# Optimization experiments

Measured on AMD Instinct MI355X. Metric: run time of the kernel, lower is better.

## Reference

```python
import jax, jax.numpy as jnp
import numpy as np

BLOCK = 8
SCALE = 0.5  # deterministic choice from scale_factors=[0.5, 0.75]


def setup_inputs() -> dict:
    key = jax.random.key(0)
    k1, k2 = jax.random.split(key)
    B, C, H, W = 32, 3, 512, 512
    x = jax.random.uniform(k1, (B, C, H, W), dtype=jnp.float32) * 2.0 - 1.0  # images in [-1,1]
    # per-8x8-block uniform values u in [0,1); noise = (u - 0.5)/50
    block_noise = jax.random.uniform(k2, (B, H // BLOCK, W // BLOCK), dtype=jnp.float32)
    return {"x": x, "block_noise": block_noise}


def reference(x, block_noise):
    B, C, H, W = x.shape
    nH, nW = int(H * SCALE), int(W * SCALE)
    # bilinear down then up, half-pixel centers == torch align_corners=False
    x_ds = jax.image.resize(x, (B, C, nH, nW), method="bilinear")
    x_rec = jax.image.resize(x_ds, (B, C, H, W), method="bilinear")
    # block noise: one scalar per 8x8 block, broadcast over channels
    noise = (block_noise - 0.5) / 50.0  # [B, H/8, W/8]
    noise_full = jnp.repeat(jnp.repeat(noise, BLOCK, axis=1), BLOCK, axis=2)  # [B, H, W]
    out = jnp.clip(x_rec + noise_full[:, None, :, :], -1.0, 1.0)
    return out
```

## Files before the change

kernel.cpp:

```cpp
#include <hip/hip_runtime.h>


typedef float f32x4 __attribute__((ext_vector_type(4)));

namespace {
constexpr int IMG = 512;
constexpr int TY = 8;
constexpr int HROWS = TY + 6;
constexpr float I32 = 1.0f / 32.0f;
constexpr float I7  = 1.0f / 7.0f;
constexpr float I28 = 1.0f / 28.0f;
}

__device__ __forceinline__ f32x4 vfma(float w, f32x4 a, f32x4 acc) {
  acc.x = fmaf(w, a.x, acc.x); acc.y = fmaf(w, a.y, acc.y);
  acc.z = fmaf(w, a.z, acc.z); acc.w = fmaf(w, a.w, acc.w);
  return acc;
}
__device__ __forceinline__ f32x4 vmul(float w, f32x4 a) {
  f32x4 r; r.x = w * a.x; r.y = w * a.y; r.z = w * a.z; r.w = w * a.w;
  return r;
}

__global__ __launch_bounds__(512) void compress_fused6_kernel(
    const float* __restrict__ x, const float* __restrict__ bn,
    float* __restrict__ out) {
  const int nwg = gridDim.x;
  const int cpx = nwg >> 3;
  const int bid = blockIdx.x;
  const int logical = (bid & 7) * cpx + (bid >> 3);
  const int ty = logical & 63;
  const int plane = logical >> 6;
  const int b = plane / 3;
  const int y0 = ty * TY;
  const int tid = threadIdx.x;
  const int cg = tid & 127;
  const int rs = tid >> 7;
  const int gx0 = 4 * cg;

  __shared__ float H[HROWS][IMG];

  const float* xp = x + (size_t)plane * (IMG * IMG);
  float* op = out + (size_t)plane * (IMG * IMG);

  const float nzv =
      (bn[(size_t)b * 4096 + (y0 >> 3) * 64 + (cg >> 1)] - 0.5f) * 0.02f;

  const bool left  = (cg == 0);
  const bool right = (cg == 127);
  const int A0 = left ? 0 : (right ? IMG - 12 : gx0 - 4);

  auto rowptr = [&](int r) -> const f32x4* {
    int g = y0 - 3 + r;
    g = max(0, min(IMG - 1, g));
    return (const f32x4*)(xp + (size_t)g * IMG + A0);
  };

  f32x4 qa, qb, qc;
  { const f32x4* p = rowptr(rs); qa = p[0]; qb = p[1]; qc = p[2]; }

#pragma unroll
  for (int k = 0; k < 4; ++k) {
    const int r = rs + 4 * k;
    const int rn = r + 4;
    f32x4 na, nb, nc;
    if (rn < HROWS) { const f32x4* p = rowptr(rn); na = p[0]; nb = p[1]; nc = p[2]; }
    if (r < HROWS) {
      const float f0 = qa.x, f1 = qa.y, f2 = qa.z, f3 = qa.w;
      const float f4_ = qb.x, f5 = qb.y, f6 = qb.z, f7 = qb.w;
      const float f8 = qc.x, f9 = qc.y, f10 = qc.z, f11 = qc.w;
      f32x4 h;
      if (left) {
        h.x = (3.f * f0 + 3.f * f1 + f2) * I7;
        h.y = 9*I28*f0 + (9*I28 + I32)*f1 + (3*I28 + 3*I32)*f2 + 3*I32*f3 + I32*f4_;
        h.z = 3*I28*f0 + (3*I28 + 3*I32)*f1 + (I28 + 9*I32)*f2 + 9*I32*f3 + 3*I32*f4_;
        h.w = (3.f*f1 + 9.f*f2 + 10.f*f3 + 6.f*f4_ + 3.f*f5 + f6) * I32;
      } else if (right) {
        h.x = (f5 + 3.f*f6 + 6.f*f7 + 10.f*f8 + 9.f*f9 + 3.f*f10) * I32;
        h.y = 3*I32*f7 + 9*I32*f8 + (I28 + 9*I32)*f9 + (3*I28 + 3*I32)*f10 + 3*I28*f11;
        h.z = I32*f7 + 3*I32*f8 + (3*I28 + 3*I32)*f9 + (9*I28 + I32)*f10 + 9*I28*f11;
        h.w = (f9 + 3.f*f10 + 3.f*f11) * I7;
      } else {
        h.x = (f1 + 3.f*f2 + 6.f*f3 + 10.f*f4_ + 9.f*f5 + 3.f*f6) * I32;
        h.y = (3.f*f3 + 9.f*f4_ + 10.f*f5 + 6.f*f6 + 3.f*f7 + f8) * I32;
        h.z = (f3 + 3.f*f4_ + 6.f*f5 + 10.f*f6 + 9.f*f7 + 3.f*f8) * I32;
        h.w = (3.f*f5 + 9.f*f6 + 10.f*f7 + 6.f*f8 + 3.f*f9 + f10) * I32;
      }
      *(f32x4*)&H[r][gx0] = h;
    }
    if (rn < HROWS) { qa = na; qb = nb; qc = nc; }
  }
  __syncthreads();

  const int wb = 2 * rs;
  const bool top = (y0 == 0);
  const bool bot = (y0 == IMG - TY);
  const int gy0 = y0 + 2 * rs;

#define LDQ(j) (*(const f32x4*)&H[wb + (j)][gx0])
  const f32x4 q0 = LDQ(0), q1 = LDQ(1), q2 = LDQ(2), q3 = LDQ(3);
  const f32x4 q4 = LDQ(4), q5 = LDQ(5), q6 = LDQ(6), q7 = LDQ(7);
#undef LDQ

  f32x4 oE, oO;
  if (top && rs == 0) {
    oE = vfma(3*I7, q3, vfma(3*I7, q4, vmul(I7, q5)));
    oO = vfma(9*I28, q3, vfma(9*I28 + I32, q4,
         vfma(3*I28 + 3*I32, q5, vfma(3*I32, q6, vmul(I32, q7)))));
  } else if (top && rs == 1) {
    oE = vfma(3*I28, q1, vfma(3*I28 + 3*I32, q2,
         vfma(I28 + 9*I32, q3, vfma(9*I32, q4, vmul(3*I32, q5)))));
    oO = vfma(3*I32, q2, vfma(9*I32, q3, vfma(10*I32, q4,
         vfma(6*I32, q5, vfma(3*I32, q6, vmul(I32, q7))))));
  } else if (bot && rs == 2) {
    oE = vfma(I32, q0, vfma(3*I32, q1, vfma(6*I32, q2,
         vfma(10*I32, q3, vfma(9*I32, q4, vmul(3*I32, q5))))));
    oO = vfma(3*I32, q2, vfma(9*I32, q3, vfma(I28 + 9*I32, q4,
         vfma(3*I28 + 3*I32, q5, vmul(3*I28, q6)))));
  } else if (bot && rs == 3) {
    oE = vfma(I32, q0, vfma(3*I32, q1, vfma(3*I28 + 3*I32, q2,
         vfma(9*I28 + I32, q3, vmul(9*I28, q4)))));
    oO = vfma(I7, q2, vfma(3*I7, q3, vmul(3*I7, q4)));
  } else {
    oE = vfma(I32, q0, vfma(3*I32, q1, vfma(6*I32, q2,
         vfma(10*I32, q3, vfma(9*I32, q4, vmul(3*I32, q5))))));
    oO = vfma(3*I32, q2, vfma(9*I32, q3, vfma(10*I32, q4,
         vfma(6*I32, q5, vfma(3*I32, q6, vmul(I32, q7))))));
  }

#define FINISH_STORE(o, ii)                                                    \
  {                                                                            \
    f32x4 v = o;                                                               \
    v.x = fminf(1.f, fmaxf(-1.f, v.x + nzv));                                  \
    v.y = fminf(1.f, fmaxf(-1.f, v.y + nzv));                                  \
    v.z = fminf(1.f, fmaxf(-1.f, v.z + nzv));                                  \
    v.w = fminf(1.f, fmaxf(-1.f, v.w + nzv));                                  \
    __builtin_nontemporal_store(v, (f32x4*)(op + (size_t)(gy0 + ii) * IMG + gx0)); \
  }
  FINISH_STORE(oE, 0)
  FINISH_STORE(oO, 1)
#undef FINISH_STORE
}

extern "C" void kernel_launch(void* const* d_in, const int* in_sizes, int n_in,
                              void* d_out, int out_size, void* d_ws, size_t ws_size,
                              hipStream_t stream) {
  const float* x  = (const float*)d_in[0];
  const float* bn = (const float*)d_in[1];
  float* out = (float*)d_out;

  const int n_planes = in_sizes[0] / (IMG * IMG);
  const int nwg = (IMG / TY) * n_planes;
  compress_fused6_kernel<<<dim3(nwg), dim3(512), 0, stream>>>(x, bn, out);
}
```

Before: 37.22 us.

## Double row tile to 16 with 1024-thread blocks and batched halo loads

Raises the output rows per workgroup from 8 to 16 and the block size from 512 to 1024 threads. The 6-row vertical halo is now amortized over twice as many output rows, which cuts redundant global reads and horizontal-pass work. The software-pipelined row loop is replaced by up to three row loads issued per thread before the horizontal convolution, and the noise index is recomputed per row group. The trade-offs are half as many workgroups, a larger shared tile, and higher register pressure under the 1024-thread launch bound.

Result: slower. 38.31 us (+2.9%).

```diff
diff --git a/kernel.cpp b/kernel.cpp
--- a/kernel.cpp
+++ b/kernel.cpp
@@ -5,7 +5,7 @@
 
 namespace {
 constexpr int IMG = 512;
-constexpr int TY = 8;
+constexpr int TY = 16;
 constexpr int HROWS = TY + 6;
 constexpr float I32 = 1.0f / 32.0f;
 constexpr float I7  = 1.0f / 7.0f;
@@ -22,15 +22,15 @@
   return r;
 }
 
-__global__ __launch_bounds__(512) void compress_fused6_kernel(
+__global__ __launch_bounds__(1024, 8) void compress_fused7_kernel(
     const float* __restrict__ x, const float* __restrict__ bn,
     float* __restrict__ out) {
   const int nwg = gridDim.x;
   const int cpx = nwg >> 3;
   const int bid = blockIdx.x;
   const int logical = (bid & 7) * cpx + (bid >> 3);
-  const int ty = logical & 63;
-  const int plane = logical >> 6;
+  const int ty = logical & 31;
+  const int plane = logical >> 5;
   const int b = plane / 3;
   const int y0 = ty * TY;
   const int tid = threadIdx.x;
@@ -44,7 +44,7 @@
   float* op = out + (size_t)plane * (IMG * IMG);
 
   const float nzv =
-      (bn[(size_t)b * 4096 + (y0 >> 3) * 64 + (cg >> 1)] - 0.5f) * 0.02f;
+      (bn[(size_t)b * 4096 + ((y0 + 2 * rs) >> 3) * 64 + (cg >> 1)] - 0.5f) * 0.02f;
 
   const bool left  = (cg == 0);
   const bool right = (cg == 127);
@@ -56,40 +56,43 @@
     return (const f32x4*)(xp + (size_t)g * IMG + A0);
   };
 
-  f32x4 qa, qb, qc;
-  { const f32x4* p = rowptr(rs); qa = p[0]; qb = p[1]; qc = p[2]; }
+  auto hconv = [&](f32x4 qa, f32x4 qb, f32x4 qc) -> f32x4 {
+    const float f0 = qa.x, f1 = qa.y, f2 = qa.z, f3 = qa.w;
+    const float f4_ = qb.x, f5 = qb.y, f6 = qb.z, f7 = qb.w;
+    const float f8 = qc.x, f9 = qc.y, f10 = qc.z, f11 = qc.w;
+    f32x4 h;
+    if (left) {
+      h.x = (3.f * f0 + 3.f * f1 + f2) * I7;
+      h.y = 9*I28*f0 + (9*I28 + I32)*f1 + (3*I28 + 3*I32)*f2 + 3*I32*f3 + I32*f4_;
+      h.z = 3*I28*f0 + (3*I28 + 3*I32)*f1 + (I28 + 9*I32)*f2 + 9*I32*f3 + 3*I32*f4_;
+      h.w = (3.f*f1 + 9.f*f2 + 10.f*f3 + 6.f*f4_ + 3.f*f5 + f6) * I32;
+    } else if (right) {
+      h.x = (f5 + 3.f*f6 + 6.f*f7 + 10.f*f8 + 9.f*f9 + 3.f*f10) * I32;
+      h.y = 3*I32*f7 + 9*I32*f8 + (I28 + 9*I32)*f9 + (3*I28 + 3*I32)*f10 + 3*I28*f11;
+      h.z = I32*f7 + 3*I32*f8 + (3*I28 + 3*I32)*f9 + (9*I28 + I32)*f10 + 9*I28*f11;
+      h.w = (f9 + 3.f*f10 + 3.f*f11) * I7;
+    } else {
+      h.x = (f1 + 3.f*f2 + 6.f*f3 + 10.f*f4_ + 9.f*f5 + 3.f*f6) * I32;
+      h.y = (3.f*f3 + 9.f*f4_ + 10.f*f5 + 6.f*f6 + 3.f*f7 + f8) * I32;
+      h.z = (f3 + 3.f*f4_ + 6.f*f5 + 10.f*f6 + 9.f*f7 + 3.f*f8) * I32;
+      h.w = (3.f*f5 + 9.f*f6 + 10.f*f7 + 6.f*f8 + 3.f*f9 + f10) * I32;
+    }
+    return h;
+  };
 
-#pragma unroll
-  for (int k = 0; k < 4; ++k) {
-    const int r = rs + 4 * k;
-    const int rn = r + 4;
-    f32x4 na, nb, nc;
-    if (rn < HROWS) { const f32x4* p = rowptr(rn); na = p[0]; nb = p[1]; nc = p[2]; }
-    if (r < HROWS) {
-      const float f0 = qa.x, f1 = qa.y, f2 = qa.z, f3 = qa.w;
-      const float f4_ = qb.x, f5 = qb.y, f6 = qb.z, f7 = qb.w;
-      const float f8 = qc.x, f9 = qc.y, f10 = qc.z, f11 = qc.w;
-      f32x4 h;
-      if (left) {
-        h.x = (3.f * f0 + 3.f * f1 + f2) * I7;
-        h.y = 9*I28*f0 + (9*I28 + I32)*f1 + (3*I28 + 3*I32)*f2 + 3*I32*f3 + I32*f4_;
-        h.z = 3*I28*f0 + (3*I28 + 3*I32)*f1 + (I28 + 9*I32)*f2 + 9*I32*f3 + 3*I32*f4_;
-        h.w = (3.f*f1 + 9.f*f2 + 10.f*f3 + 6.f*f4_ + 3.f*f5 + f6) * I32;
-      } else if (right) {
-        h.x = (f5 + 3.f*f6 + 6.f*f7 + 10.f*f8 + 9.f*f9 + 3.f*f10) * I32;
-        h.y = 3*I32*f7 + 9*I32*f8 + (I28 + 9*I32)*f9 + (3*I28 + 3*I32)*f10 + 3*I28*f11;
-        h.z = I32*f7 + 3*I32*f8 + (3*I28 + 3*I32)*f9 + (9*I28 + I32)*f10 + 9*I28*f11;
-        h.w = (f9 + 3.f*f10 + 3.f*f11) * I7;
-      } else {
-        h.x = (f1 + 3.f*f2 + 6.f*f3 + 10.f*f4_ + 9.f*f5 + 3.f*f6) * I32;
-        h.y = (3.f*f3 + 9.f*f4_ + 10.f*f5 + 6.f*f6 + 3.f*f7 + f8) * I32;
-        h.z = (f3 + 3.f*f4_ + 6.f*f5 + 10.f*f6 + 9.f*f7 + 3.f*f8) * I32;
-        h.w = (3.f*f5 + 9.f*f6 + 10.f*f7 + 6.f*f8 + 3.f*f9 + f10) * I32;
-      }
-      *(f32x4*)&H[r][gx0] = h;
-    }
-    if (rn < HROWS) { qa = na; qb = nb; qc = nc; }
-  }
+  const bool has2 = (rs < 6);
+  const f32x4* p0 = rowptr(rs);
+  const f32x4* p1 = rowptr(rs + 8);
+  f32x4 a0 = p0[0], b0 = p0[1], c0 = p0[2];
+  f32x4 a1 = p1[0], b1 = p1[1], c1 = p1[2];
+
+  *(f32x4*)&H[rs][gx0] = hconv(a0, b0, c0);
+
+  f32x4 a2, b2, c2;
+  if (has2) { const f32x4* p2 = rowptr(rs + 16); a2 = p2[0]; b2 = p2[1]; c2 = p2[2]; }
+
+  *(f32x4*)&H[rs + 8][gx0] = hconv(a1, b1, c1);
+  if (has2) *(f32x4*)&H[rs + 16][gx0] = hconv(a2, b2, c2);
   __syncthreads();
 
   const int wb = 2 * rs;
@@ -112,12 +115,12 @@
          vfma(I28 + 9*I32, q3, vfma(9*I32, q4, vmul(3*I32, q5)))));
     oO = vfma(3*I32, q2, vfma(9*I32, q3, vfma(10*I32, q4,
          vfma(6*I32, q5, vfma(3*I32, q6, vmul(I32, q7))))));
-  } else if (bot && rs == 2) {
+  } else if (bot && rs == 6) {
     oE = vfma(I32, q0, vfma(3*I32, q1, vfma(6*I32, q2,
          vfma(10*I32, q3, vfma(9*I32, q4, vmul(3*I32, q5))))));
     oO = vfma(3*I32, q2, vfma(9*I32, q3, vfma(I28 + 9*I32, q4,
          vfma(3*I28 + 3*I32, q5, vmul(3*I28, q6)))));
-  } else if (bot && rs == 3) {
+  } else if (bot && rs == 7) {
     oE = vfma(I32, q0, vfma(3*I32, q1, vfma(3*I28 + 3*I32, q2,
          vfma(9*I28 + I32, q3, vmul(9*I28, q4)))));
     oO = vfma(I7, q2, vfma(3*I7, q3, vmul(3*I7, q4)));
@@ -151,5 +154,5 @@
 
   const int n_planes = in_sizes[0] / (IMG * IMG);
   const int nwg = (IMG / TY) * n_planes;
-  compress_fused6_kernel<<<dim3(nwg), dim3(512), 0, stream>>>(x, bn, out);
+  compress_fused7_kernel<<<dim3(nwg), dim3(1024), 0, stream>>>(x, bn, out);
 }
```

## Replace shared-memory tile with per-thread register sliding window over 16-row strips

Applied to the files above, without the earlier changes.

Each workgroup now has 128 threads that walk a 16-row strip, holding the horizontal-filter results in registers as a sliding window. This replaces the 8-row tile staged in LDS behind a barrier. The halo overhead drops from 6 extra rows per 8 to 6 per 16, and the shared memory and __syncthreads go away. Loads are software-pipelined through a 4-slot register ring. The trade-offs are fewer workgroups, higher register pressure, a longer serial dependency per thread, and a switch from nontemporal to regular stores.

Measured after the change: 40.26 us. +8.2%, slower.

```diff
diff --git a/kernel.cpp b/kernel.cpp
--- a/kernel.cpp
+++ b/kernel.cpp
@@ -5,8 +5,7 @@
 
 namespace {
 constexpr int IMG = 512;
-constexpr int TY = 8;
-constexpr int HROWS = TY + 6;
+constexpr int TY = 16;
 constexpr float I32 = 1.0f / 32.0f;
 constexpr float I7  = 1.0f / 7.0f;
 constexpr float I28 = 1.0f / 28.0f;
@@ -22,123 +21,132 @@
   return r;
 }
 
-__global__ __launch_bounds__(512) void compress_fused6_kernel(
+__global__ __launch_bounds__(128, 4) void compress_fused12_kernel(
     const float* __restrict__ x, const float* __restrict__ bn,
     float* __restrict__ out) {
-  const int nwg = gridDim.x;
-  const int cpx = nwg >> 3;
   const int bid = blockIdx.x;
-  const int logical = (bid & 7) * cpx + (bid >> 3);
-  const int ty = logical & 63;
-  const int plane = logical >> 6;
+  const int sid = (bid & 7) * (gridDim.x >> 3) + (bid >> 3);
+  const int plane = sid >> 5;
+  const int st = sid & 31;
+  const int y0 = st * TY;
   const int b = plane / 3;
-  const int y0 = ty * TY;
-  const int tid = threadIdx.x;
-  const int cg = tid & 127;
-  const int rs = tid >> 7;
+  const int cg = threadIdx.x;
   const int gx0 = 4 * cg;
-
-  __shared__ float H[HROWS][IMG];
 
   const float* xp = x + (size_t)plane * (IMG * IMG);
   float* op = out + (size_t)plane * (IMG * IMG);
 
-  const float nzv =
-      (bn[(size_t)b * 4096 + (y0 >> 3) * 64 + (cg >> 1)] - 0.5f) * 0.02f;
+  const float nz0 = (bn[(size_t)b * 4096 + (2 * st) * 64 + (cg >> 1)] - 0.5f) * 0.02f;
+  const float nz1 = (bn[(size_t)b * 4096 + (2 * st + 1) * 64 + (cg >> 1)] - 0.5f) * 0.02f;
 
   const bool left  = (cg == 0);
   const bool right = (cg == 127);
   const int A0 = left ? 0 : (right ? IMG - 12 : gx0 - 4);
 
-  auto rowptr = [&](int r) -> const f32x4* {
-    int g = y0 - 3 + r;
+  f32x4 buf[4][3];
+  f32x4 h[8];
+
+  auto LOAD = [&](int j, int s) {
+    int g = y0 - 3 + j;
     g = max(0, min(IMG - 1, g));
-    return (const f32x4*)(xp + (size_t)g * IMG + A0);
+    const f32x4* p = (const f32x4*)(xp + (size_t)g * IMG + A0);
+    buf[s][0] = p[0]; buf[s][1] = p[1]; buf[s][2] = p[2];
   };
 
-  f32x4 qa, qb, qc;
-  { const f32x4* p = rowptr(rs); qa = p[0]; qb = p[1]; qc = p[2]; }
+  auto hconv = [&](const f32x4& qa, const f32x4& qb, const f32x4& qc) -> f32x4 {
+    const float f0 = qa.x, f1 = qa.y, f2 = qa.z, f3 = qa.w;
+    const float f4_ = qb.x, f5 = qb.y, f6 = qb.z, f7 = qb.w;
+    const float f8 = qc.x, f9 = qc.y, f10 = qc.z, f11 = qc.w;
+    f32x4 r;
+    if (left) {
+      r.x = (3.f * f0 + 3.f * f1 + f2) * I7;
+      r.y = 9*I28*f0 + (9*I28 + I32)*f1 + (3*I28 + 3*I32)*f2 + 3*I32*f3 + I32*f4_;
+      r.z = 3*I28*f0 + (3*I28 + 3*I32)*f1 + (I28 + 9*I32)*f2 + 9*I32*f3 + 3*I32*f4_;
+      r.w = (3.f*f1 + 9.f*f2 + 10.f*f3 + 6.f*f4_ + 3.f*f5 + f6) * I32;
+    } else if (right) {
+      r.x = (f5 + 3.f*f6 + 6.f*f7 + 10.f*f8 + 9.f*f9 + 3.f*f10) * I32;
+      r.y = 3*I32*f7 + 9*I32*f8 + (I28 + 9*I32)*f9 + (3*I28 + 3*I32)*f10 + 3*I28*f11;
+      r.z = I32*f7 + 3*I32*f8 + (3*I28 + 3*I32)*f9 + (9*I28 + I32)*f10 + 9*I28*f11;
+      r.w = (f9 + 3.f*f10 + 3.f*f11) * I7;
+    } else {
+      r.x = (f1 + 3.f*f2 + 6.f*f3 + 10.f*f4_ + 9.f*f5 + 3.f*f6) * I32;
+      r.y = (3.f*f3 + 9.f*f4_ + 10.f*f5 + 6.f*f6 + 3.f*f7 + f8) * I32;
+      r.z = (f3 + 3.f*f4_ + 6.f*f5 + 10.f*f6 + 9.f*f7 + 3.f*f8) * I32;
+      r.w = (3.f*f5 + 9.f*f6 + 10.f*f7 + 6.f*f8 + 3.f*f9 + f10) * I32;
+    }
+    return r;
+  };
+
+  LOAD(0, 0) ; LOAD(1, 1); LOAD(2, 2); LOAD(3, 3);
+  h[0] = hconv(buf[0][0], buf[0][1], buf[0][2]);
+  h[1] = hconv(buf[1][0], buf[1][1], buf[1][2]);
+  LOAD(4, 0); LOAD(5, 1);
+  h[2] = hconv(buf[2][0], buf[2][1], buf[2][2]);
+  h[3] = hconv(buf[3][0], buf[3][1], buf[3][2]);
+  LOAD(6, 2); LOAD(7, 3);
+  h[4] = hconv(buf[0][0], buf[0][1], buf[0][2]);
+  h[5] = hconv(buf[1][0], buf[1][1], buf[1][2]);
+  LOAD(8, 0); LOAD(9, 1);
+  h[6] = hconv(buf[2][0], buf[2][1], buf[2][2]);
+  h[7] = hconv(buf[3][0], buf[3][1], buf[3][2]);
+
+#define FINISH_STORE(o, gy, NZ)                                                \
+  {                                                                            \
+    f32x4 v = o;                                                               \
+    v.x = fminf(1.f, fmaxf(-1.f, v.x + NZ));                                   \
+    v.y = fminf(1.f, fmaxf(-1.f, v.y + NZ));                                   \
+    v.z = fminf(1.f, fmaxf(-1.f, v.z + NZ));                                   \
+    v.w = fminf(1.f, fmaxf(-1.f, v.w + NZ));                                   \
+    *(f32x4*)(op + (size_t)(gy) * IMG + gx0) = v;                              \
+  }
 
 #pragma unroll
-  for (int k = 0; k < 4; ++k) {
-    const int r = rs + 4 * k;
-    const int rn = r + 4;
-    f32x4 na, nb, nc;
-    if (rn < HROWS) { const f32x4* p = rowptr(rn); na = p[0]; nb = p[1]; nc = p[2]; }
-    if (r < HROWS) {
-      const float f0 = qa.x, f1 = qa.y, f2 = qa.z, f3 = qa.w;
-      const float f4_ = qb.x, f5 = qb.y, f6 = qb.z, f7 = qb.w;
-      const float f8 = qc.x, f9 = qc.y, f10 = qc.z, f11 = qc.w;
-      f32x4 h;
-      if (left) {
-        h.x = (3.f * f0 + 3.f * f1 + f2) * I7;
-        h.y = 9*I28*f0 + (9*I28 + I32)*f1 + (3*I28 + 3*I32)*f2 + 3*I32*f3 + I32*f4_;
-        h.z = 3*I28*f0 + (3*I28 + 3*I32)*f1 + (I28 + 9*I32)*f2 + 9*I32*f3 + 3*I32*f4_;
-        h.w = (3.f*f1 + 9.f*f2 + 10.f*f3 + 6.f*f4_ + 3.f*f5 + f6) * I32;
-      } else if (right) {
-        h.x = (f5 + 3.f*f6 + 6.f*f7 + 10.f*f8 + 9.f*f9 + 3.f*f10) * I32;
-        h.y = 3*I32*f7 + 9*I32*f8 + (I28 + 9*I32)*f9 + (3*I28 + 3*I32)*f10 + 3*I28*f11;
-        h.z = I32*f7 + 3*I32*f8 + (3*I28 + 3*I32)*f9 + (9*I28 + I32)*f10 + 9*I28*f11;
-        h.w = (f9 + 3.f*f10 + 3.f*f11) * I7;
+  for (int t = 0; t < 8; ++t) {
+    const float nzv = (t < 4) ? nz0 : nz1;
+    const int gy = y0 + 2 * t;
+    f32x4 oE, oO;
+    if (st == 0 && t == 0) {
+      oE = vfma(3*I7, h[3], vfma(3*I7, h[4], vmul(I7, h[5])));
+      oO = vfma(9*I28, h[3], vfma(9*I28 + I32, h[4],
+           vfma(3*I28 + 3*I32, h[5], vfma(3*I32, h[6], vmul(I32, h[7])))));
+    } else if (st == 0 && t == 1) {
+      oE = vfma(3*I28, h[1], vfma(3*I28 + 3*I32, h[2],
+           vfma(I28 + 9*I32, h[3], vfma(9*I32, h[4], vmul(3*I32, h[5])))));
+      oO = vfma(3*I32, h[2], vfma(9*I32, h[3], vfma(10*I32, h[4],
+           vfma(6*I32, h[5], vfma(3*I32, h[6], vmul(I32, h[7]))))));
+    } else if (st == 31 && t == 6) {
+      oE = vfma(I32, h[0], vfma(3*I32, h[1], vfma(6*I32, h[2],
+           vfma(10*I32, h[3], vfma(9*I32, h[4], vmul(3*I32, h[5]))))));
+      oO = vfma(3*I32, h[2], vfma(9*I32, h[3], vfma(I28 + 9*I32, h[4],
+           vfma(3*I28 + 3*I32, h[5], vmul(3*I28, h[6])))));
+    } else if (st == 31 && t == 7) {
+      oE = vfma(I32, h[0], vfma(3*I32, h[1], vfma(3*I28 + 3*I32, h[2],
+           vfma(9*I28 + I32, h[3], vmul(9*I28, h[4])))));
+      oO = vfma(I7, h[2], vfma(3*I7, h[3], vmul(3*I7, h[4])));
+    } else {
+      oE = vfma(I32, h[0], vfma(3*I32, h[1], vfma(6*I32, h[2],
+           vfma(10*I32, h[3], vfma(9*I32, h[4], vmul(3*I32, h[5]))))));
+      oO = vfma(3*I32, h[2], vfma(9*I32, h[3], vfma(10*I32, h[4],
+           vfma(6*I32, h[5], vfma(3*I32, h[6], vmul(I32, h[7]))))));
+    }
+    FINISH_STORE(oE, gy, nzv)
+    FINISH_STORE(oO, gy + 1, nzv)
+
+    if (t < 7) {
+      if (t < 6) {
+        if ((t & 1) == 0) { LOAD(2 * t + 10, 2); LOAD(2 * t + 11, 3); }
+        else              { LOAD(2 * t + 10, 0); LOAD(2 * t + 11, 1); }
+      }
+      h[0] = h[2]; h[1] = h[3]; h[2] = h[4]; h[3] = h[5]; h[4] = h[6]; h[5] = h[7];
+      if ((t & 1) == 0) {
+        h[6] = hconv(buf[0][0], buf[0][1], buf[0][2]);
+        h[7] = hconv(buf[1][0], buf[1][1], buf[1][2]);
       } else {
-        h.x = (f1 + 3.f*f2 + 6.f*f3 + 10.f*f4_ + 9.f*f5 + 3.f*f6) * I32;
-        h.y = (3.f*f3 + 9.f*f4_ + 10.f*f5 + 6.f*f6 + 3.f*f7 + f8) * I32;
-        h.z = (f3 + 3.f*f4_ + 6.f*f5 + 10.f*f6 + 9.f*f7 + 3.f*f8) * I32;
-        h.w = (3.f*f5 + 9.f*f6 + 10.f*f7 + 6.f*f8 + 3.f*f9 + f10) * I32;
+        h[6] = hconv(buf[2][0], buf[2][1], buf[2][2]);
+        h[7] = hconv(buf[3][0], buf[3][1], buf[3][2]);
       }
-      *(f32x4*)&H[r][gx0] = h;
     }
-    if (rn < HROWS) { qa = na; qb = nb; qc = nc; }
   }
-  __syncthreads();
-
-  const int wb = 2 * rs;
-  const bool top = (y0 == 0);
-  const bool bot = (y0 == IMG - TY);
-  const int gy0 = y0 + 2 * rs;
-
-#define LDQ(j) (*(const f32x4*)&H[wb + (j)][gx0])
-  const f32x4 q0 = LDQ(0), q1 = LDQ(1), q2 = LDQ(2), q3 = LDQ(3);
-  const f32x4 q4 = LDQ(4), q5 = LDQ(5), q6 = LDQ(6), q7 = LDQ(7);
-#undef LDQ
-
-  f32x4 oE, oO;
-  if (top && rs == 0) {
-    oE = vfma(3*I7, q3, vfma(3*I7, q4, vmul(I7, q5)));
-    oO = vfma(9*I28, q3, vfma(9*I28 + I32, q4,
-         vfma(3*I28 + 3*I32, q5, vfma(3*I32, q6, vmul(I32, q7)))));
-  } else if (top && rs == 1) {
-    oE = vfma(3*I28, q1, vfma(3*I28 + 3*I32, q2,
-         vfma(I28 + 9*I32, q3, vfma(9*I32, q4, vmul(3*I32, q5)))));
-    oO = vfma(3*I32, q2, vfma(9*I32, q3, vfma(10*I32, q4,
-         vfma(6*I32, q5, vfma(3*I32, q6, vmul(I32, q7))))));
-  } else if (bot && rs == 2) {
-    oE = vfma(I32, q0, vfma(3*I32, q1, vfma(6*I32, q2,
-         vfma(10*I32, q3, vfma(9*I32, q4, vmul(3*I32, q5))))));
-    oO = vfma(3*I32, q2, vfma(9*I32, q3, vfma(I28 + 9*I32, q4,
-         vfma(3*I28 + 3*I32, q5, vmul(3*I28, q6)))));
-  } else if (bot && rs == 3) {
-    oE = vfma(I32, q0, vfma(3*I32, q1, vfma(3*I28 + 3*I32, q2,
-         vfma(9*I28 + I32, q3, vmul(9*I28, q4)))));
-    oO = vfma(I7, q2, vfma(3*I7, q3, vmul(3*I7, q4)));
-  } else {
-    oE = vfma(I32, q0, vfma(3*I32, q1, vfma(6*I32, q2,
-         vfma(10*I32, q3, vfma(9*I32, q4, vmul(3*I32, q5))))));
-    oO = vfma(3*I32, q2, vfma(9*I32, q3, vfma(10*I32, q4,
-         vfma(6*I32, q5, vfma(3*I32, q6, vmul(I32, q7))))));
-  }
-
-#define FINISH_STORE(o, ii)                                                    \
-  {                                                                            \
-    f32x4 v = o;                                                               \
-    v.x = fminf(1.f, fmaxf(-1.f, v.x + nzv));                                  \
-    v.y = fminf(1.f, fmaxf(-1.f, v.y + nzv));                                  \
-    v.z = fminf(1.f, fmaxf(-1.f, v.z + nzv));                                  \
-    v.w = fminf(1.f, fmaxf(-1.f, v.w + nzv));                                  \
-    __builtin_nontemporal_store(v, (f32x4*)(op + (size_t)(gy0 + ii) * IMG + gx0)); \
-  }
-  FINISH_STORE(oE, 0)
-  FINISH_STORE(oO, 1)
 #undef FINISH_STORE
 }
 
@@ -151,5 +159,5 @@
 
   const int n_planes = in_sizes[0] / (IMG * IMG);
   const int nwg = (IMG / TY) * n_planes;
-  compress_fused6_kernel<<<dim3(nwg), dim3(512), 0, stream>>>(x, bn, out);
+  compress_fused12_kernel<<<dim3(nwg), dim3(128), 0, stream>>>(x, bn, out);
 }
```
